# Kernel optimization log

Measured on AMD Instinct MI355X. Metric: run time of the kernel, lower is better.

The kernel has to match this reference:

```python
import jax, jax.numpy as jnp
from jax import lax
import numpy as np

SMOOTH = 0.015
EPS = 1e-9


def setup_inputs() -> dict:
    key = jax.random.key(0)
    k_x, k_a, k_p, k_b = jax.random.split(key, 4)
    B, F, T, C = 64, 256, 2048, 1
    x = jax.random.uniform(k_x, (B, F, T, C), dtype=jnp.float32)  # nonneg energies
    # learned scalars ~ N(1.0, 0.1) as in tf.random_normal_initializer(mean=1.0, stddev=0.1)
    alpha = 1.0 + 0.1 * jax.random.normal(k_a, (1,), dtype=jnp.float32)
    power = 1.0 + 0.1 * jax.random.normal(k_p, (1,), dtype=jnp.float32)
    bias = 1.0 + 0.1 * jax.random.normal(k_b, (1,), dtype=jnp.float32)
    return {"x": x, "alpha": alpha, "power": power, "bias": bias}


def _smoother(x):
    # x: [B, F, T, C]; IIR: M_0 = s*x_0, M_t = (1-s)*M_{t-1} + s*x_t
    xt = jnp.moveaxis(x, 2, 0)  # [T, B, F, C]
    m0 = SMOOTH * xt[0]

    def step(m_prev, xi):
        m = (1.0 - SMOOTH) * m_prev + SMOOTH * xi
        return m, m

    _, ms = lax.scan(step, m0, xt[1:])
    M = jnp.concatenate([m0[None], ms], axis=0)  # [T, B, F, C]
    return jnp.moveaxis(M, 0, 2)  # [B, F, T, C]


def reference(x, alpha, power, bias):
    M = _smoother(x)
    return jnp.power(x / jnp.power(EPS + M, alpha) + bias, power) - jnp.power(bias, power)
```

## Files before the change

kernel.cpp:

```cpp
#include <hip/hip_runtime.h>


#define T_LEN      2048
#define PAD_STRIDE 33
#define LDS_ROW    (64 * PAD_STRIDE)

__device__ __forceinline__ float fast_exp2(float x) { return __builtin_amdgcn_exp2f(x); }
__device__ __forceinline__ float fast_log2(float x) { return __builtin_amdgcn_logf(x); }

__global__ __launch_bounds__(256) void pcen_kernel(
    const float* __restrict__ x,
    const float* __restrict__ alpha_p,
    const float* __restrict__ power_p,
    const float* __restrict__ bias_p,
    float* __restrict__ out)
{
    __shared__ float lds[4][LDS_ROW];

    const int wave = threadIdx.x >> 6;
    const int lane = threadIdx.x & 63;
    const int row  = (blockIdx.x << 2) | wave;

    const float alpha = alpha_p[0];
    const float power = power_p[0];
    const float bias  = bias_p[0];

    const float A = 0.985f;
    const float S = 0.015f;

    const float* xr  = x   + (size_t)row * T_LEN;
    float*       orw = out + (size_t)row * T_LEN;
    float*       L   = lds[wave];

#pragma unroll
    for (int k = 0; k < 8; ++k) {
        const int e = 4 * lane + 256 * k;
        const float4 v = *reinterpret_cast<const float4*>(xr + e);
        const int idx = ((e >> 5) * PAD_STRIDE) + (e & 31);
        L[idx + 0] = v.x; L[idx + 1] = v.y; L[idx + 2] = v.z; L[idx + 3] = v.w;
    }
    __syncthreads();

    float xv[32], mv[32];
    const int base = lane * PAD_STRIDE;
    float m = 0.0f;
#pragma unroll
    for (int j = 0; j < 32; ++j) {
        const float xx = L[base + j];
        xv[j] = xx;
        m = A * m + S * xx;
        mv[j] = m;
    }

    float f = A; f *= f; f *= f; f *= f; f *= f; f *= f;
    float s = m;
    float g = f;
#pragma unroll
    for (int d = 1; d < 64; d <<= 1) {
        const float so = __shfl_up(s, d, 64);
        if (lane >= d) s += g * so;
        g *= g;
    }
    float carry = __shfl_up(s, 1, 64);
    if (lane == 0) carry = 0.0f;

    const float bias_pow = fast_exp2(power * fast_log2(bias));
    float pa = A * carry;
#pragma unroll
    for (int j = 0; j < 32; ++j) {
        const float M   = mv[j] + pa;
        pa *= A;
        const float den = 1e-9f + M;
        const float t   = xv[j] * fast_exp2(-alpha * fast_log2(den)) + bias;
        const float r   = fast_exp2(power * fast_log2(t)) - bias_pow;
        L[base + j] = r;
    }
    __syncthreads();

#pragma unroll
    for (int k = 0; k < 8; ++k) {
        const int e   = 4 * lane + 256 * k;
        const int idx = ((e >> 5) * PAD_STRIDE) + (e & 31);
        float4 v;
        v.x = L[idx + 0]; v.y = L[idx + 1]; v.z = L[idx + 2]; v.w = L[idx + 3];
        *reinterpret_cast<float4*>(orw + e) = v;
    }
}

extern "C" void kernel_launch(void* const* d_in, const int* in_sizes, int n_in,
                              void* d_out, int out_size, void* d_ws, size_t ws_size,
                              hipStream_t stream) {
    const float* x       = (const float*)d_in[0];
    const float* alpha_p = (const float*)d_in[1];
    const float* power_p = (const float*)d_in[2];
    const float* bias_p  = (const float*)d_in[3];
    float* out           = (float*)d_out;

    const int nrows  = in_sizes[0] / T_LEN;
    const int blocks = nrows / 4;

    pcen_kernel<<<blocks, 256, 0, stream>>>(x, alpha_p, power_p, bias_p, out);
}
```

Baseline: 238.0 us.

## Drop LDS transpose; scan register-resident float4 chunks with per-chunk wave scans

Each lane now keeps its coalesced float4 loads in registers instead of transposing the row through padded LDS. The recurrence is split into 8 chunks of 256 elements per wave, each solved with a wave-wide shuffle scan, and a carry is passed between chunks using A^(4*lane) and A^256. This removes the LDS stores and loads and the two block barriers. In exchange it issues eight times as many shuffles and computes the decay factor through exp2/log2, which may lose some precision.

```diff
diff --git a/kernel.cpp b/kernel.cpp
--- a/kernel.cpp
+++ b/kernel.cpp
@@ -1,9 +1,7 @@
 #include <hip/hip_runtime.h>
 
 
-#define T_LEN      2048
-#define PAD_STRIDE 33
-#define LDS_ROW    (64 * PAD_STRIDE)
+#define T_LEN 2048
 
 __device__ __forceinline__ float fast_exp2(float x) { return __builtin_amdgcn_exp2f(x); }
 __device__ __forceinline__ float fast_log2(float x) { return __builtin_amdgcn_logf(x); }
@@ -15,8 +13,6 @@
     const float* __restrict__ bias_p,
     float* __restrict__ out)
 {
-    __shared__ float lds[4][LDS_ROW];
-
     const int wave = threadIdx.x >> 6;
     const int lane = threadIdx.x & 63;
     const int row  = (blockIdx.x << 2) | wave;
@@ -30,60 +26,62 @@
 
     const float* xr  = x   + (size_t)row * T_LEN;
     float*       orw = out + (size_t)row * T_LEN;
-    float*       L   = lds[wave];
 
+    float4 xv[8];
+#pragma unroll
+    for (int k = 0; k < 8; ++k)
+        xv[k] = *reinterpret_cast<const float4*>(xr + 4 * lane + 256 * k);
+
+    float s[8];
 #pragma unroll
     for (int k = 0; k < 8; ++k) {
-        const int e = 4 * lane + 256 * k;
-        const float4 v = *reinterpret_cast<const float4*>(xr + e);
-        const int idx = ((e >> 5) * PAD_STRIDE) + (e & 31);
-        L[idx + 0] = v.x; L[idx + 1] = v.y; L[idx + 2] = v.z; L[idx + 3] = v.w;
-    }
-    __syncthreads();
-
-    float xv[32], mv[32];
-    const int base = lane * PAD_STRIDE;
-    float m = 0.0f;
-#pragma unroll
-    for (int j = 0; j < 32; ++j) {
-        const float xx = L[base + j];
-        xv[j] = xx;
-        m = A * m + S * xx;
-        mv[j] = m;
+        float m = 0.0f;
+        m = A * m + S * xv[k].x;
+        m = A * m + S * xv[k].y;
+        m = A * m + S * xv[k].z;
+        m = A * m + S * xv[k].w;
+        s[k] = m;
     }
 
-    float f = A; f *= f; f *= f; f *= f; f *= f; f *= f;
-    float s = m;
-    float g = f;
+    float g = A; g *= g; g *= g;
 #pragma unroll
     for (int d = 1; d < 64; d <<= 1) {
-        const float so = __shfl_up(s, d, 64);
-        if (lane >= d) s += g * so;
+#pragma unroll
+        for (int k = 0; k < 8; ++k) {
+            const float so = __shfl_up(s[k], d, 64);
+            if (lane >= d) s[k] += g * so;
+        }
         g *= g;
     }
-    float carry = __shfl_up(s, 1, 64);
-    if (lane == 0) carry = 0.0f;
+
+    const float log2A = fast_log2(A);
+    const float A4L   = fast_exp2((float)(4 * lane) * log2A);
+    float A256 = A; 
+#pragma unroll
+    for (int i = 0; i < 8; ++i) A256 *= A256;
 
     const float bias_pow = fast_exp2(power * fast_log2(bias));
-    float pa = A * carry;
-#pragma unroll
-    for (int j = 0; j < 32; ++j) {
-        const float M   = mv[j] + pa;
-        pa *= A;
-        const float den = 1e-9f + M;
-        const float t   = xv[j] * fast_exp2(-alpha * fast_log2(den)) + bias;
-        const float r   = fast_exp2(power * fast_log2(t)) - bias_pow;
-        L[base + j] = r;
-    }
-    __syncthreads();
 
+    float C = 0.0f;
 #pragma unroll
     for (int k = 0; k < 8; ++k) {
-        const int e   = 4 * lane + 256 * k;
-        const int idx = ((e >> 5) * PAD_STRIDE) + (e & 31);
-        float4 v;
-        v.x = L[idx + 0]; v.y = L[idx + 1]; v.z = L[idx + 2]; v.w = L[idx + 3];
-        *reinterpret_cast<float4*>(orw + e) = v;
+        float excl = __shfl_up(s[k], 1, 64);
+        if (lane == 0) excl = 0.0f;
+        const float endk = __shfl(s[k], 63, 64);
+
+        float m = excl + A4L * C;
+        float4 o;
+#pragma unroll
+        for (int j = 0; j < 4; ++j) {
+            const float xx = (&xv[k].x)[j];
+            m = A * m + S * xx;
+            const float den = 1e-9f + m;
+            const float t   = xx * fast_exp2(-alpha * fast_log2(den)) + bias;
+            (&o.x)[j] = fast_exp2(power * fast_log2(t)) - bias_pow;
+        }
+        *reinterpret_cast<float4*>(orw + 4 * lane + 256 * k) = o;
+
+        C = endk + A256 * C;
     }
 }
 
```

Result: no change. 239.0 us (+0.4%).
